# Optimization experiments

Measured on AMD Instinct MI355X. Metric: run time of the kernel, lower is better.

Reference implementation:

```python
import jax, jax.numpy as jnp
import numpy as np

N, n, m, k = 100000, 32, 16, 32
MU = 100.0  # bubble kernel scale (init arg mu)


def setup_inputs() -> dict:
    key = jax.random.key(0)
    ks = jax.random.split(key, 7)
    x = jax.random.normal(ks[0], (N,), dtype=jnp.float32)
    # torch.nn.Linear(N, n): weight [n, N], bias [n]
    encoder_w = jax.random.normal(ks[1], (n, N), dtype=jnp.float32) / np.float32(np.sqrt(N))
    encoder_b = jnp.zeros((n,), dtype=jnp.float32)
    # decoder parameter [n, N]
    decoder = jax.random.normal(ks[2], (n, N), dtype=jnp.float32) / np.float32(np.sqrt(n))
    # torch.nn.Linear(n, n*m): weight [n*m, n], bias [n*m]
    bw_w = jax.random.normal(ks[3], (n * m, n), dtype=jnp.float32) / np.float32(np.sqrt(n))
    bw_b = jnp.zeros((n * m,), dtype=jnp.float32)
    neighbour_distance = jax.random.uniform(ks[4], (N, k), dtype=jnp.float32)
    neighbour_id = jax.random.randint(ks[5], (N, k), 0, N)
    clustering_labels = jax.random.randint(ks[6], (N,), 0, m)
    return {
        "x": x,
        "encoder_w": encoder_w,
        "encoder_b": encoder_b,
        "decoder": decoder,
        "bw_w": bw_w,
        "bw_b": bw_b,
        "neighbour_distance": neighbour_distance,
        "neighbour_id": neighbour_id,
        "clustering_labels": clustering_labels,
    }


def reference(x, encoder_w, encoder_b, decoder, bw_w, bw_b,
              neighbour_distance, neighbour_id, clustering_labels):
    # encode: [N] -> [n]
    encoded = x @ encoder_w.T + encoder_b
    # per-basis, per-cluster bandwidths: sigmoid(Linear)/60 -> [n, m] -> expand to [n, N]
    bandwidths = jax.nn.sigmoid(encoded @ bw_w.T + bw_b) / 60.0
    w = bandwidths.reshape(n, m)[:, clustering_labels]  # [n, N]
    # bubble window: relu(1 - d^2 / (w*mu)^2) -> [n, N, k]
    window = jax.nn.relu(1.0 - neighbour_distance[None, :, :] ** 2
                         / (w[:, :, None] * MU) ** 2)
    # normalization over axis 1 (the N axis), faithful to the source's dim=1
    window = window / jnp.sum(window, axis=1, keepdims=True)
    # gather decoder rows at neighbours, weight, reduce over k: [n, N]
    convolved_basis = jnp.sum(decoder[:, neighbour_id] * window, axis=-1)
    # [n] @ [n, N] -> [N]
    return encoded @ convolved_basis
```

## Files before the change

kernel.cpp:

```cpp
#include <hip/hip_runtime.h>
#include <hip/hip_fp16.h>

#define N_PTS 100000
#define MU_F  100.0f
#define BUCKET 8192

typedef unsigned int uint;
typedef _Float16 h2 __attribute__((ext_vector_type(2)));
typedef float f2 __attribute__((ext_vector_type(2)));

#define E_SCALE 16384.0f
#define E_SCALE_INV (1.0f / 16384.0f)

static __device__ inline h2 h2pack(float a, float b) {
    return __builtin_bit_cast(h2, __builtin_amdgcn_cvt_pkrtz(a, b));
}
static __device__ inline float fdot2f(h2 a, h2 b, float c) {
    return __builtin_amdgcn_fdot2(a, b, c, false);
}
static __device__ inline h2 h2fma(h2 a, h2 b, h2 c) {
#if __has_builtin(__builtin_elementwise_fma)
    return __builtin_elementwise_fma(a, b, c);
#else
    return a * b + c;
#endif
}
static __device__ inline h2 h2max(h2 a, h2 b) {
#if __has_builtin(__builtin_elementwise_max)
    return __builtin_elementwise_max(a, b);
#else
    h2 r;
    r.x = a.x > b.x ? a.x : b.x;
    r.y = a.y > b.y ? a.y : b.y;
    return r;
#endif
}

#define ENC_BLKS 256
#define SC_BLKS  98
#define TR_BLKS  1563
#define S_BLKS   1024

__global__ __launch_bounds__(256) void k_prep(const float* __restrict__ x,
                                              const float* __restrict__ encW,
                                              const float* __restrict__ encB,
                                              const int* __restrict__ labels,
                                              float* __restrict__ enc,
                                              int* __restrict__ gcur,
                                              int* __restrict__ perm) {
    int b = blockIdx.x;
    if (b < ENC_BLKS) {
        int row = b & 31;
        int chunk = b >> 5;
        const int CH = N_PTS / 8;
        int base = chunk * CH;
        const float4* W4 = reinterpret_cast<const float4*>(encW + (size_t)row * N_PTS + base);
        const float4* x4 = reinterpret_cast<const float4*>(x + base);
        const int nv = CH / 4;
        float acc = 0.f;
        for (int idx = threadIdx.x; idx < nv; idx += 256) {
            float4 w = W4[idx];
            float4 xv = x4[idx];
            acc += w.x * xv.x + w.y * xv.y + w.z * xv.z + w.w * xv.w;
        }
        #pragma unroll
        for (int off = 32; off > 0; off >>= 1) acc += __shfl_down(acc, off);
        __shared__ float sred[4];
        int wid = threadIdx.x >> 6;
        if ((threadIdx.x & 63) == 0) sred[wid] = acc;
        __syncthreads();
        if (threadIdx.x == 0) {
            float s = sred[0] + sred[1] + sred[2] + sred[3];
            if (chunk == 0) s += encB[row];
            atomicAdd(enc + row, s);
        }
    } else {
        __shared__ int lh[16], lbase[16], lcur[16];
        const int CHUNK = 1024;
        int start = (b - ENC_BLKS) * CHUNK;
        int end = min(start + CHUNK, N_PTS);
        if (threadIdx.x < 16) { lh[threadIdx.x] = 0; lcur[threadIdx.x] = 0; }
        __syncthreads();
        for (int j = start + threadIdx.x; j < end; j += 256)
            atomicAdd(&lh[labels[j]], 1);
        __syncthreads();
        if (threadIdx.x < 16)
            lbase[threadIdx.x] = threadIdx.x * BUCKET +
                                 atomicAdd(&gcur[threadIdx.x], lh[threadIdx.x]);
        __syncthreads();
        for (int j = start + threadIdx.x; j < end; j += 256) {
            int c = labels[j];
            int lpos = atomicAdd(&lcur[c], 1);
            perm[lbase[c] + lpos] = j;
        }
    }
}

__device__ inline void build_invC(const float* __restrict__ encL,
                                  const float* __restrict__ bw_w,
                                  const float* __restrict__ bw_b,
                                  float* __restrict__ invCL, int c) {
    if (threadIdx.x < 32) {
        int r = threadIdx.x * 16 + c;
        float z = bw_b[r];
        const float* wr = bw_w + r * 32;
        #pragma unroll
        for (int p = 0; p < 32; ++p) z = fmaf(encL[p], wr[p], z);
        float s = 1.f / (1.f + __expf(-z));
        float wmu = s * (MU_F / 60.0f);
        invCL[threadIdx.x] = 1.f / (wmu * wmu);
    }
}

__global__ __launch_bounds__(256, 4) void k_S_sorted(const float* __restrict__ enc_g,
                                                     const float* __restrict__ bw_w,
                                                     const float* __restrict__ bw_b,
                                                     const float* __restrict__ nd,
                                                     const int* __restrict__ perm,
                                                     const int* __restrict__ gcur,
                                                     float* __restrict__ S,
                                                     float* __restrict__ S_part,
                                                     const float* __restrict__ dec,
                                                     __half* __restrict__ decT) {
    int b = blockIdx.x;
    if (b >= S_BLKS) {
        __shared__ float tile[32][65];
        int j0 = (b - S_BLKS) * 64;
        int col = threadIdx.x & 63;
        int r0 = threadIdx.x >> 6;
        #pragma unroll
        for (int it = 0; it < 8; ++it) {
            int row = it * 4 + r0;
            int j = j0 + col;
            float v = (j < N_PTS) ? dec[(size_t)row * N_PTS + j] : 0.f;
            tile[row][col] = v;
        }
        __syncthreads();
        #pragma unroll
        for (int it = 0; it < 4; ++it) {
            int idx = it * 256 + threadIdx.x;
            int j = idx >> 4;
            int p = idx & 15;
            int jj = j0 + j;
            if (jj < N_PTS) {
                __half2 h = __halves2half2(__float2half(tile[2 * p][j]),
                                           __float2half(tile[2 * p + 1][j]));
                *reinterpret_cast<__half2*>(decT + (size_t)jj * 32 + 2 * p) = h;
            }
        }
        return;
    }

    __shared__ float encL[32], invCL[32];
    __shared__ float Sloc[1024];
    int c = b & 15;
    int ch = b >> 4;
    if (threadIdx.x < 32) encL[threadIdx.x] = enc_g[threadIdx.x];
    for (int t = threadIdx.x; t < 1024; t += 256) Sloc[t] = 0.f;
    __syncthreads();
    build_invC(encL, bw_w, bw_b, invCL, c);
    __syncthreads();

    f2 inv2[16];
    #pragma unroll
    for (int t = 0; t < 16; ++t) { inv2[t].x = invCL[2 * t]; inv2[t].y = invCL[2 * t + 1]; }

    int bs = c * BUCKET;
    int cnt = gcur[c];
    int lane = threadIdx.x & 63;
    int kk = lane & 31;
    int jh = lane >> 5;
    int gw = ch * 4 + (threadIdx.x >> 6);
    const int nw = 64 * 4;
    int npairs = (cnt + 1) >> 1;

    f2 acc2[16];
    #pragma unroll
    for (int t = 0; t < 16; ++t) { acc2[t].x = 0.f; acc2[t].y = 0.f; }

    if (gw < npairs) {
        auto ld = [&](int pc, float& d, bool& v) {
            bool ok = pc < npairs;
            v = ok && (2 * pc + jh) < cnt;
            int p = v ? (bs + 2 * pc + jh) : bs;
            int j = __builtin_nontemporal_load(&perm[p]);
            d = __builtin_nontemporal_load(&nd[(size_t)j * 32 + kk]);
        };
        int pp = gw;
        float dA, dB; bool vA, vB;
        ld(pp, dA, vA);
        ld(pp + nw, dB, vB);
        while (pp < npairs) {
            float dC; bool vC;
            ld(pp + 2 * nw, dC, vC);
            float d2 = vA ? dA * dA : 1e30f;
            f2 md2; md2.x = -d2; md2.y = -d2;
            f2 onev; onev.x = 1.f; onev.y = 1.f;
            #pragma unroll
            for (int t = 0; t < 16; ++t) {
                f2 w = md2 * inv2[t] + onev;
                w.x = fmaxf(w.x, 0.f);
                w.y = fmaxf(w.y, 0.f);
                acc2[t] += w;
            }
            dA = dB; vA = vB; dB = dC; vB = vC;
            pp += nw;
        }
    }
    #pragma unroll
    for (int t = 0; t < 16; ++t) {
        acc2[t].x += __shfl_xor(acc2[t].x, 32);
        acc2[t].y += __shfl_xor(acc2[t].y, 32);
    }
    if (jh == 0) {
        #pragma unroll
        for (int t = 0; t < 16; ++t) {
            atomicAdd(&Sloc[(2 * t) * 32 + kk], acc2[t].x);
            atomicAdd(&Sloc[(2 * t + 1) * 32 + kk], acc2[t].y);
        }
    }
    __syncthreads();
    if (S_part) {
        for (int t = threadIdx.x; t < 1024; t += 256)
            S_part[(size_t)b * 1024 + t] = Sloc[t];
    } else {
        for (int t = threadIdx.x; t < 1024; t += 256) {
            float v = Sloc[t];
            if (v != 0.f) atomicAdd(&S[t], v);
        }
    }
}

__global__ __launch_bounds__(1024) void k_S_reduce(const float* __restrict__ S_part,
                                                   float* __restrict__ S) {
    int g = blockIdx.x;
    int t = threadIdx.x;
    float s = 0.f;
    #pragma unroll
    for (int u = 0; u < 16; ++u)
        s += S_part[(size_t)(g * 16 + u) * 1024 + t];
    atomicAdd(&S[t], s);
}

__global__ __launch_bounds__(256, 4) void k_main(const float* __restrict__ enc_g,
                                                 const float* __restrict__ bw_w,
                                                 const float* __restrict__ bw_b,
                                                 const float* __restrict__ S_g,
                                                 const float* __restrict__ nd,
                                                 const int* __restrict__ nid,
                                                 const int* __restrict__ perm,
                                                 const int* __restrict__ gcur,
                                                 const __half* __restrict__ decT,
                                                 float* __restrict__ out) {
    __shared__ float encL[32], invCL[32];
    __shared__ float ELf[1024];
    int c = blockIdx.x & 15;
    int ch = blockIdx.x >> 4;
    if (threadIdx.x < 32) encL[threadIdx.x] = enc_g[threadIdx.x];
    __syncthreads();
    build_invC(encL, bw_w, bw_b, invCL, c);
    for (int t = threadIdx.x; t < 1024; t += 256)
        ELf[t] = encL[t >> 5] / S_g[t] * E_SCALE;
    __syncthreads();

    int lane = threadIdx.x & 63;
    int R = lane >> 2;
    int q = lane & 3;

    h2 invh[4], EhA[4], EhB[4];
    #pragma unroll
    for (int t = 0; t < 4; ++t) {
        int i0 = q * 8 + 2 * t;
        invh[t] = h2pack(fminf(invCL[i0], 6.0e4f), fminf(invCL[i0 + 1], 6.0e4f));
        EhA[t] = h2pack(ELf[i0 * 32 + R], ELf[(i0 + 1) * 32 + R]);
        EhB[t] = h2pack(ELf[i0 * 32 + R + 16], ELf[(i0 + 1) * 32 + R + 16]);
    }
    const h2 zero2 = h2pack(0.f, 0.f);
    const h2 one2 = h2pack(1.f, 1.f);

    int bs = c * BUCKET;
    int cnt = gcur[c];
    int wv = ch * 4 + (threadIdx.x >> 6);
    const int NW = 64 * 4;
    int npairs = (cnt + 1) >> 1;
    const uint4* decQ = reinterpret_cast<const uint4*>(decT);
    if (wv >= npairs) return;

    auto load_pair = [&](int pp, int& j0, int& j1, bool& v1) {
        bool ok = pp < npairs;
        int p0 = ok ? (bs + 2 * pp) : bs;
        v1 = ok && ((2 * pp + 1) < cnt);
        j0 = perm[p0];
        j1 = perm[v1 ? p0 + 1 : p0];
    };
    auto load_ids = [&](int j0, int j1, int* id, float* dd) {
        #pragma unroll
        for (int s = 0; s < 4; ++s) {
            int jj = (s >> 1) ? j1 : j0;
            size_t idx = (size_t)jj * 32 + (s & 1) * 16 + R;
            id[s] = __builtin_nontemporal_load(&nid[idx]);
            dd[s] = __builtin_nontemporal_load(&nd[idx]);
        }
    };
    auto load_rows = [&](const int* id, uint4* r) {
        #pragma unroll
        for (int s = 0; s < 4; ++s)
            r[s] = decQ[(size_t)id[s] * 4 + q];
    };

    int pp = wv;
    int j0a, j1a, j0b, j1b, j0c, j1c; bool v1a, v1b, v1c;
    int ida[4], idn[4]; float dda[4], ddn[4];
    uint4 ra[4], rb[4];

    load_pair(pp, j0a, j1a, v1a);
    load_ids(j0a, j1a, ida, dda);
    load_pair(pp + NW, j0b, j1b, v1b);
    load_rows(ida, ra);
    load_ids(j0b, j1b, idn, ddn);
    load_pair(pp + 2 * NW, j0c, j1c, v1c);

    while (pp < npairs) {
        load_rows(idn, rb);
        int idc[4]; float ddc[4];
        load_ids(j0c, j1c, idc, ddc);
        int j0d, j1d; bool v1d;
        load_pair(pp + 3 * NW, j0d, j1d, v1d);

        float d20 = dda[0] * dda[0];
        float d21 = dda[1] * dda[1];
        float d22 = dda[2] * dda[2];
        float d23 = dda[3] * dda[3];
        h2 md0 = h2pack(-d20, -d20);
        h2 md1 = h2pack(-d21, -d21);
        h2 md2 = h2pack(-d22, -d22);
        h2 md3 = h2pack(-d23, -d23);

        float a0 = 0.f, a1 = 0.f, a2 = 0.f, a3 = 0.f;
        #pragma unroll
        for (int t = 0; t < 4; ++t) {
            uint dw0 = (t == 0) ? ra[0].x : (t == 1) ? ra[0].y : (t == 2) ? ra[0].z : ra[0].w;
            uint dw1 = (t == 0) ? ra[1].x : (t == 1) ? ra[1].y : (t == 2) ? ra[1].z : ra[1].w;
            uint dw2 = (t == 0) ? ra[2].x : (t == 1) ? ra[2].y : (t == 2) ? ra[2].z : ra[2].w;
            uint dw3 = (t == 0) ? ra[3].x : (t == 1) ? ra[3].y : (t == 2) ? ra[3].z : ra[3].w;
            {
                h2 w = h2max(h2fma(md0, invh[t], one2), zero2);
                a0 = fdot2f(w * EhA[t], __builtin_bit_cast(h2, dw0), a0);
            }
            {
                h2 w = h2max(h2fma(md1, invh[t], one2), zero2);
                a1 = fdot2f(w * EhB[t], __builtin_bit_cast(h2, dw1), a1);
            }
            {
                h2 w = h2max(h2fma(md2, invh[t], one2), zero2);
                a2 = fdot2f(w * EhA[t], __builtin_bit_cast(h2, dw2), a2);
            }
            {
                h2 w = h2max(h2fma(md3, invh[t], one2), zero2);
                a3 = fdot2f(w * EhB[t], __builtin_bit_cast(h2, dw3), a3);
            }
        }
        float u = a0 + a1;
        float v = a2 + a3;
        #pragma unroll
        for (int off = 32; off > 0; off >>= 1) {
            u += __shfl_xor(u, off);
            v += __shfl_xor(v, off);
        }
        if (lane == 0) out[j0a] = u * E_SCALE_INV;
        if (lane == 32 && v1a) out[j1a] = v * E_SCALE_INV;

        j0a = j0b; j1a = j1b; v1a = v1b;
        j0b = j0c; j1b = j1c; v1b = v1c;
        j0c = j0d; j1c = j1d; v1c = v1d;
        #pragma unroll
        for (int s = 0; s < 4; ++s) {
            dda[s] = ddn[s];
            ddn[s] = ddc[s];
            idn[s] = idc[s];
            ra[s] = rb[s];
        }
        pp += NW;
    }
}

extern "C" void kernel_launch(void* const* d_in, const int* in_sizes, int n_in,
                              void* d_out, int out_size, void* d_ws, size_t ws_size,
                              hipStream_t stream) {
    const float* x     = (const float*)d_in[0];
    const float* enc_w = (const float*)d_in[1];
    const float* enc_b = (const float*)d_in[2];
    const float* dec   = (const float*)d_in[3];
    const float* bw_w  = (const float*)d_in[4];
    const float* bw_b  = (const float*)d_in[5];
    const float* nd    = (const float*)d_in[6];
    const int*   nid   = (const int*)d_in[7];
    const int*   labels= (const int*)d_in[8];
    float* out = (float*)d_out;

    char* ws = (char*)d_ws;
    float* enc    = (float*)(ws + 0);
    float* S      = (float*)(ws + 128);
    int* gcur     = (int*)(ws + 4224);
    int* perm     = (int*)(ws + 8192);
    __half* decT  = (__half*)(ws + 532480);
    bool use_part = ws_size >= 11126784ull;
    float* S_part = use_part ? (float*)(ws + 6932480) : nullptr;

    (void)hipMemsetAsync(d_ws, 0, 4288, stream);
    k_prep<<<dim3(ENC_BLKS + SC_BLKS), dim3(256), 0, stream>>>(
        x, enc_w, enc_b, labels, enc, gcur, perm);
    k_S_sorted<<<dim3(S_BLKS + TR_BLKS), dim3(256), 0, stream>>>(
        enc, bw_w, bw_b, nd, perm, gcur, S, S_part, dec, decT);
    if (use_part)
        k_S_reduce<<<dim3(64), dim3(1024), 0, stream>>>(S_part, S);
    k_main<<<dim3(1024), dim3(256), 0, stream>>>(enc, bw_w, bw_b, S, nd, nid,
                                                 perm, gcur, decT, out);
}
```

Measured before the change: 180.2 us.

## Drop cluster-label sort; index per-point bandwidths from shared table in natural order

Removes the counting-sort permutation by cluster label and its per-bucket work distribution. Both the S-reduction and the main kernel now walk points in their natural order in contiguous chunks, and they look up each point's inverse bandwidths from a 16x32 shared-memory table indexed by label. This gets rid of the perm indirection, the sort work in k_prep and the label-imbalanced buckets, and makes the nd/nid loads contiguous. The cost is per-point shared-memory table reads that depend on the label, plus the full 512-entry bandwidth computation in every block.

```diff
diff --git a/kernel.cpp b/kernel.cpp
--- a/kernel.cpp
+++ b/kernel.cpp
@@ -3,7 +3,6 @@
 
 #define N_PTS 100000
 #define MU_F  100.0f
-#define BUCKET 8192
 
 typedef unsigned int uint;
 typedef _Float16 h2 __attribute__((ext_vector_type(2)));
@@ -37,91 +36,69 @@
 }
 
 #define ENC_BLKS 256
-#define SC_BLKS  98
 #define TR_BLKS  1563
 #define S_BLKS   1024
+#define NPAIRS   (N_PTS / 2)
+#define S_CH     ((NPAIRS + S_BLKS - 1) / S_BLKS)
+#define M_BLKS   1024
+#define M_CH     ((NPAIRS + M_BLKS - 1) / M_BLKS)
 
 __global__ __launch_bounds__(256) void k_prep(const float* __restrict__ x,
                                               const float* __restrict__ encW,
                                               const float* __restrict__ encB,
-                                              const int* __restrict__ labels,
-                                              float* __restrict__ enc,
-                                              int* __restrict__ gcur,
-                                              int* __restrict__ perm) {
+                                              float* __restrict__ enc) {
     int b = blockIdx.x;
-    if (b < ENC_BLKS) {
-        int row = b & 31;
-        int chunk = b >> 5;
-        const int CH = N_PTS / 8;
-        int base = chunk * CH;
-        const float4* W4 = reinterpret_cast<const float4*>(encW + (size_t)row * N_PTS + base);
-        const float4* x4 = reinterpret_cast<const float4*>(x + base);
-        const int nv = CH / 4;
-        float acc = 0.f;
-        for (int idx = threadIdx.x; idx < nv; idx += 256) {
-            float4 w = W4[idx];
-            float4 xv = x4[idx];
-            acc += w.x * xv.x + w.y * xv.y + w.z * xv.z + w.w * xv.w;
-        }
-        #pragma unroll
-        for (int off = 32; off > 0; off >>= 1) acc += __shfl_down(acc, off);
-        __shared__ float sred[4];
-        int wid = threadIdx.x >> 6;
-        if ((threadIdx.x & 63) == 0) sred[wid] = acc;
-        __syncthreads();
-        if (threadIdx.x == 0) {
-            float s = sred[0] + sred[1] + sred[2] + sred[3];
-            if (chunk == 0) s += encB[row];
-            atomicAdd(enc + row, s);
-        }
-    } else {
-        __shared__ int lh[16], lbase[16], lcur[16];
-        const int CHUNK = 1024;
-        int start = (b - ENC_BLKS) * CHUNK;
-        int end = min(start + CHUNK, N_PTS);
-        if (threadIdx.x < 16) { lh[threadIdx.x] = 0; lcur[threadIdx.x] = 0; }
-        __syncthreads();
-        for (int j = start + threadIdx.x; j < end; j += 256)
-            atomicAdd(&lh[labels[j]], 1);
-        __syncthreads();
-        if (threadIdx.x < 16)
-            lbase[threadIdx.x] = threadIdx.x * BUCKET +
-                                 atomicAdd(&gcur[threadIdx.x], lh[threadIdx.x]);
-        __syncthreads();
-        for (int j = start + threadIdx.x; j < end; j += 256) {
-            int c = labels[j];
-            int lpos = atomicAdd(&lcur[c], 1);
-            perm[lbase[c] + lpos] = j;
-        }
-    }
-}
-
-__device__ inline void build_invC(const float* __restrict__ encL,
+    int row = b & 31;
+    int chunk = b >> 5;
+    const int CH = N_PTS / 8;
+    int base = chunk * CH;
+    const float4* W4 = reinterpret_cast<const float4*>(encW + (size_t)row * N_PTS + base);
+    const float4* x4 = reinterpret_cast<const float4*>(x + base);
+    const int nv = CH / 4;
+    float acc = 0.f;
+    for (int idx = threadIdx.x; idx < nv; idx += 256) {
+        float4 w = W4[idx];
+        float4 xv = x4[idx];
+        acc += w.x * xv.x + w.y * xv.y + w.z * xv.z + w.w * xv.w;
+    }
+    #pragma unroll
+    for (int off = 32; off > 0; off >>= 1) acc += __shfl_down(acc, off);
+    __shared__ float sred[4];
+    int wid = threadIdx.x >> 6;
+    if ((threadIdx.x & 63) == 0) sred[wid] = acc;
+    __syncthreads();
+    if (threadIdx.x == 0) {
+        float s = sred[0] + sred[1] + sred[2] + sred[3];
+        if (chunk == 0) s += encB[row];
+        atomicAdd(enc + row, s);
+    }
+}
+
+__device__ inline void build_invF(const float* __restrict__ encL,
                                   const float* __restrict__ bw_w,
                                   const float* __restrict__ bw_b,
-                                  float* __restrict__ invCL, int c) {
-    if (threadIdx.x < 32) {
-        int r = threadIdx.x * 16 + c;
+                                  float* __restrict__ invF) {
+    for (int r = threadIdx.x; r < 512; r += 256) {
+        int i = r >> 4, c = r & 15;
         float z = bw_b[r];
         const float* wr = bw_w + r * 32;
         #pragma unroll
         for (int p = 0; p < 32; ++p) z = fmaf(encL[p], wr[p], z);
         float s = 1.f / (1.f + __expf(-z));
         float wmu = s * (MU_F / 60.0f);
-        invCL[threadIdx.x] = 1.f / (wmu * wmu);
-    }
-}
-
-__global__ __launch_bounds__(256, 4) void k_S_sorted(const float* __restrict__ enc_g,
-                                                     const float* __restrict__ bw_w,
-                                                     const float* __restrict__ bw_b,
-                                                     const float* __restrict__ nd,
-                                                     const int* __restrict__ perm,
-                                                     const int* __restrict__ gcur,
-                                                     float* __restrict__ S,
-                                                     float* __restrict__ S_part,
-                                                     const float* __restrict__ dec,
-                                                     __half* __restrict__ decT) {
+        invF[c * 32 + i] = 1.f / (wmu * wmu);
+    }
+}
+
+__global__ __launch_bounds__(256, 4) void k_S(const float* __restrict__ enc_g,
+                                              const float* __restrict__ bw_w,
+                                              const float* __restrict__ bw_b,
+                                              const float* __restrict__ nd,
+                                              const int* __restrict__ labels,
+                                              float* __restrict__ S,
+                                              float* __restrict__ S_part,
+                                              const float* __restrict__ dec,
+                                              __half* __restrict__ decT) {
     int b = blockIdx.x;
     if (b >= S_BLKS) {
         __shared__ float tile[32][65];
@@ -151,60 +128,60 @@
         return;
     }
 
-    __shared__ float encL[32], invCL[32];
+    __shared__ float encL[32];
+    __shared__ float invF[512];
     __shared__ float Sloc[1024];
-    int c = b & 15;
-    int ch = b >> 4;
     if (threadIdx.x < 32) encL[threadIdx.x] = enc_g[threadIdx.x];
     for (int t = threadIdx.x; t < 1024; t += 256) Sloc[t] = 0.f;
     __syncthreads();
-    build_invC(encL, bw_w, bw_b, invCL, c);
-    __syncthreads();
-
-    f2 inv2[16];
-    #pragma unroll
-    for (int t = 0; t < 16; ++t) { inv2[t].x = invCL[2 * t]; inv2[t].y = invCL[2 * t + 1]; }
-
-    int bs = c * BUCKET;
-    int cnt = gcur[c];
+    build_invF(encL, bw_w, bw_b, invF);
+    __syncthreads();
+
     int lane = threadIdx.x & 63;
     int kk = lane & 31;
     int jh = lane >> 5;
-    int gw = ch * 4 + (threadIdx.x >> 6);
-    const int nw = 64 * 4;
-    int npairs = (cnt + 1) >> 1;
+    int w = threadIdx.x >> 6;
+    int start = b * S_CH;
+    int pend = min(start + S_CH, NPAIRS);
+    int p = start + w;
 
     f2 acc2[16];
     #pragma unroll
     for (int t = 0; t < 16; ++t) { acc2[t].x = 0.f; acc2[t].y = 0.f; }
 
-    if (gw < npairs) {
-        auto ld = [&](int pc, float& d, bool& v) {
-            bool ok = pc < npairs;
-            v = ok && (2 * pc + jh) < cnt;
-            int p = v ? (bs + 2 * pc + jh) : bs;
-            int j = __builtin_nontemporal_load(&perm[p]);
-            d = __builtin_nontemporal_load(&nd[(size_t)j * 32 + kk]);
+    if (p < pend) {
+        auto ld = [&](int pc, float& d, int& c) {
+            pc = min(pc, NPAIRS - 1);
+            int j = 2 * pc + jh;
+            d = nd[(size_t)j * 32 + kk];
+            c = labels[j];
         };
-        int pp = gw;
-        float dA, dB; bool vA, vB;
-        ld(pp, dA, vA);
-        ld(pp + nw, dB, vB);
-        while (pp < npairs) {
-            float dC; bool vC;
-            ld(pp + 2 * nw, dC, vC);
-            float d2 = vA ? dA * dA : 1e30f;
+        float dA, dB; int cA, cB;
+        ld(p, dA, cA);
+        ld(p + 4, dB, cB);
+        f2 onev; onev.x = 1.f; onev.y = 1.f;
+        while (p < pend) {
+            float dC; int cC;
+            ld(p + 8, dC, cC);
+            float d2 = dA * dA;
             f2 md2; md2.x = -d2; md2.y = -d2;
-            f2 onev; onev.x = 1.f; onev.y = 1.f;
+            const float4* ivp = reinterpret_cast<const float4*>(&invF[cA * 32]);
             #pragma unroll
-            for (int t = 0; t < 16; ++t) {
-                f2 w = md2 * inv2[t] + onev;
-                w.x = fmaxf(w.x, 0.f);
-                w.y = fmaxf(w.y, 0.f);
-                acc2[t] += w;
-            }
-            dA = dB; vA = vB; dB = dC; vB = vC;
-            pp += nw;
+            for (int t4 = 0; t4 < 8; ++t4) {
+                float4 iv = ivp[t4];
+                f2 i01; i01.x = iv.x; i01.y = iv.y;
+                f2 i23; i23.x = iv.z; i23.y = iv.w;
+                f2 w0 = md2 * i01 + onev;
+                w0.x = fmaxf(w0.x, 0.f);
+                w0.y = fmaxf(w0.y, 0.f);
+                acc2[2 * t4] += w0;
+                f2 w1 = md2 * i23 + onev;
+                w1.x = fmaxf(w1.x, 0.f);
+                w1.y = fmaxf(w1.y, 0.f);
+                acc2[2 * t4 + 1] += w1;
+            }
+            dA = dB; cA = cB; dB = dC; cB = cC;
+            p += 4;
         }
     }
     #pragma unroll
@@ -248,84 +225,92 @@
                                                  const float* __restrict__ S_g,
                                                  const float* __restrict__ nd,
                                                  const int* __restrict__ nid,
-                                                 const int* __restrict__ perm,
-                                                 const int* __restrict__ gcur,
+                                                 const int* __restrict__ labels,
                                                  const __half* __restrict__ decT,
                                                  float* __restrict__ out) {
-    __shared__ float encL[32], invCL[32];
+    __shared__ float encL[32];
+    __shared__ float invF[512];
     __shared__ float ELf[1024];
-    int c = blockIdx.x & 15;
-    int ch = blockIdx.x >> 4;
+    __shared__ h2 invHL[256];
+
     if (threadIdx.x < 32) encL[threadIdx.x] = enc_g[threadIdx.x];
     __syncthreads();
-    build_invC(encL, bw_w, bw_b, invCL, c);
+    build_invF(encL, bw_w, bw_b, invF);
     for (int t = threadIdx.x; t < 1024; t += 256)
         ELf[t] = encL[t >> 5] / S_g[t] * E_SCALE;
+    __syncthreads();
+    {
+        int t = threadIdx.x;
+        int c = t >> 4, q = (t >> 2) & 3, tt = t & 3;
+        int i0 = q * 8 + 2 * tt;
+        invHL[t] = h2pack(fminf(invF[c * 32 + i0], 6.0e4f),
+                          fminf(invF[c * 32 + i0 + 1], 6.0e4f));
+    }
     __syncthreads();
 
     int lane = threadIdx.x & 63;
     int R = lane >> 2;
     int q = lane & 3;
 
-    h2 invh[4], EhA[4], EhB[4];
+    h2 EhA[4], EhB[4];
     #pragma unroll
     for (int t = 0; t < 4; ++t) {
         int i0 = q * 8 + 2 * t;
-        invh[t] = h2pack(fminf(invCL[i0], 6.0e4f), fminf(invCL[i0 + 1], 6.0e4f));
         EhA[t] = h2pack(ELf[i0 * 32 + R], ELf[(i0 + 1) * 32 + R]);
         EhB[t] = h2pack(ELf[i0 * 32 + R + 16], ELf[(i0 + 1) * 32 + R + 16]);
     }
     const h2 zero2 = h2pack(0.f, 0.f);
     const h2 one2 = h2pack(1.f, 1.f);
 
-    int bs = c * BUCKET;
-    int cnt = gcur[c];
-    int wv = ch * 4 + (threadIdx.x >> 6);
-    const int NW = 64 * 4;
-    int npairs = (cnt + 1) >> 1;
+    int w = threadIdx.x >> 6;
+    int start = blockIdx.x * M_CH;
+    int pend = min(start + M_CH, NPAIRS);
+    int pa = start + w;
     const uint4* decQ = reinterpret_cast<const uint4*>(decT);
-    if (wv >= npairs) return;
-
-    auto load_pair = [&](int pp, int& j0, int& j1, bool& v1) {
-        bool ok = pp < npairs;
-        int p0 = ok ? (bs + 2 * pp) : bs;
-        v1 = ok && ((2 * pp + 1) < cnt);
-        j0 = perm[p0];
-        j1 = perm[v1 ? p0 + 1 : p0];
-    };
-    auto load_ids = [&](int j0, int j1, int* id, float* dd) {
+    if (pa >= pend) return;
+
+    auto load_ldd = [&](int pc, int* id, float* dd, int& c0, int& c1) {
+        pc = min(pc, NPAIRS - 1);
+        int j0 = 2 * pc, j1 = j0 + 1;
         #pragma unroll
         for (int s = 0; s < 4; ++s) {
-            int jj = (s >> 1) ? j1 : j0;
-            size_t idx = (size_t)jj * 32 + (s & 1) * 16 + R;
-            id[s] = __builtin_nontemporal_load(&nid[idx]);
-            dd[s] = __builtin_nontemporal_load(&nd[idx]);
-        }
+            size_t idx = (size_t)((s >> 1) ? j1 : j0) * 32 + (s & 1) * 16 + R;
+            id[s] = nid[idx];
+            dd[s] = nd[idx];
+        }
+        c0 = labels[j0];
+        c1 = labels[j1];
     };
     auto load_rows = [&](const int* id, uint4* r) {
         #pragma unroll
         for (int s = 0; s < 4; ++s)
             r[s] = decQ[(size_t)id[s] * 4 + q];
     };
-
-    int pp = wv;
-    int j0a, j1a, j0b, j1b, j0c, j1c; bool v1a, v1b, v1c;
-    int ida[4], idn[4]; float dda[4], ddn[4];
+    auto load_ih = [&](int c0, int c1, h2* ih0, h2* ih1) {
+        uint4 a = *reinterpret_cast<const uint4*>(&invHL[c0 * 16 + q * 4]);
+        uint4 bq = *reinterpret_cast<const uint4*>(&invHL[c1 * 16 + q * 4]);
+        ih0[0] = __builtin_bit_cast(h2, a.x);  ih0[1] = __builtin_bit_cast(h2, a.y);
+        ih0[2] = __builtin_bit_cast(h2, a.z);  ih0[3] = __builtin_bit_cast(h2, a.w);
+        ih1[0] = __builtin_bit_cast(h2, bq.x); ih1[1] = __builtin_bit_cast(h2, bq.y);
+        ih1[2] = __builtin_bit_cast(h2, bq.z); ih1[3] = __builtin_bit_cast(h2, bq.w);
+    };
+
+    int ida[4], idb[4]; float dda[4], ddb[4];
+    int ca0, ca1, cb0, cb1;
     uint4 ra[4], rb[4];
-
-    load_pair(pp, j0a, j1a, v1a);
-    load_ids(j0a, j1a, ida, dda);
-    load_pair(pp + NW, j0b, j1b, v1b);
+    h2 ihA0[4], ihA1[4];
+
+    load_ldd(pa, ida, dda, ca0, ca1);
+    load_ldd(pa + 4, idb, ddb, cb0, cb1);
     load_rows(ida, ra);
-    load_ids(j0b, j1b, idn, ddn);
-    load_pair(pp + 2 * NW, j0c, j1c, v1c);
-
-    while (pp < npairs) {
-        load_rows(idn, rb);
-        int idc[4]; float ddc[4];
-        load_ids(j0c, j1c, idc, ddc);
-        int j0d, j1d; bool v1d;
-        load_pair(pp + 3 * NW, j0d, j1d, v1d);
+    load_ih(ca0, ca1, ihA0, ihA1);
+
+    while (pa < pend) {
+        load_rows(idb, rb);
+        h2 ihB0[4], ihB1[4];
+        load_ih(cb0, cb1, ihB0, ihB1);
+        int idc[4]; float ddc[4]; int cc0, cc1;
+        load_ldd(pa + 8, idc, ddc, cc0, cc1);
 
         float d20 = dda[0] * dda[0];
         float d21 = dda[1] * dda[1];
@@ -344,20 +329,20 @@
             uint dw2 = (t == 0) ? ra[2].x : (t == 1) ? ra[2].y : (t == 2) ? ra[2].z : ra[2].w;
             uint dw3 = (t == 0) ? ra[3].x : (t == 1) ? ra[3].y : (t == 2) ? ra[3].z : ra[3].w;
             {
-                h2 w = h2max(h2fma(md0, invh[t], one2), zero2);
-                a0 = fdot2f(w * EhA[t], __builtin_bit_cast(h2, dw0), a0);
+                h2 wv = h2max(h2fma(md0, ihA0[t], one2), zero2);
+                a0 = fdot2f(wv * EhA[t], __builtin_bit_cast(h2, dw0), a0);
             }
             {
-                h2 w = h2max(h2fma(md1, invh[t], one2), zero2);
-                a1 = fdot2f(w * EhB[t], __builtin_bit_cast(h2, dw1), a1);
+                h2 wv = h2max(h2fma(md1, ihA0[t], one2), zero2);
+                a1 = fdot2f(wv * EhB[t], __builtin_bit_cast(h2, dw1), a1);
             }
             {
-                h2 w = h2max(h2fma(md2, invh[t], one2), zero2);
-                a2 = fdot2f(w * EhA[t], __builtin_bit_cast(h2, dw2), a2);
+                h2 wv = h2max(h2fma(md2, ihA1[t], one2), zero2);
+                a2 = fdot2f(wv * EhA[t], __builtin_bit_cast(h2, dw2), a2);
             }
             {
-                h2 w = h2max(h2fma(md3, invh[t], one2), zero2);
-                a3 = fdot2f(w * EhB[t], __builtin_bit_cast(h2, dw3), a3);
+                h2 wv = h2max(h2fma(md3, ihA1[t], one2), zero2);
+                a3 = fdot2f(wv * EhB[t], __builtin_bit_cast(h2, dw3), a3);
             }
         }
         float u = a0 + a1;
@@ -367,20 +352,18 @@
             u += __shfl_xor(u, off);
             v += __shfl_xor(v, off);
         }
-        if (lane == 0) out[j0a] = u * E_SCALE_INV;
-        if (lane == 32 && v1a) out[j1a] = v * E_SCALE_INV;
-
-        j0a = j0b; j1a = j1b; v1a = v1b;
-        j0b = j0c; j1b = j1c; v1b = v1c;
-        j0c = j0d; j1c = j1d; v1c = v1d;
+        if (lane == 0)  out[2 * pa]     = u * E_SCALE_INV;
+        if (lane == 32) out[2 * pa + 1] = v * E_SCALE_INV;
+
+        ca0 = cb0; ca1 = cb1; cb0 = cc0; cb1 = cc1;
         #pragma unroll
         for (int s = 0; s < 4; ++s) {
-            dda[s] = ddn[s];
-            ddn[s] = ddc[s];
-            idn[s] = idc[s];
+            dda[s] = ddb[s]; ddb[s] = ddc[s];
+            ida[s] = idb[s]; idb[s] = idc[s];
             ra[s] = rb[s];
-        }
-        pp += NW;
+            ihA0[s] = ihB0[s]; ihA1[s] = ihB1[s];
+        }
+        pa += 4;
     }
 }
 
@@ -401,19 +384,16 @@
     char* ws = (char*)d_ws;
     float* enc    = (float*)(ws + 0);
     float* S      = (float*)(ws + 128);
-    int* gcur     = (int*)(ws + 4224);
-    int* perm     = (int*)(ws + 8192);
     __half* decT  = (__half*)(ws + 532480);
     bool use_part = ws_size >= 11126784ull;
     float* S_part = use_part ? (float*)(ws + 6932480) : nullptr;
 
-    (void)hipMemsetAsync(d_ws, 0, 4288, stream);
-    k_prep<<<dim3(ENC_BLKS + SC_BLKS), dim3(256), 0, stream>>>(
-        x, enc_w, enc_b, labels, enc, gcur, perm);
-    k_S_sorted<<<dim3(S_BLKS + TR_BLKS), dim3(256), 0, stream>>>(
-        enc, bw_w, bw_b, nd, perm, gcur, S, S_part, dec, decT);
+    (void)hipMemsetAsync(d_ws, 0, 4224, stream);
+    k_prep<<<dim3(ENC_BLKS), dim3(256), 0, stream>>>(x, enc_w, enc_b, enc);
+    k_S<<<dim3(S_BLKS + TR_BLKS), dim3(256), 0, stream>>>(
+        enc, bw_w, bw_b, nd, labels, S, S_part, dec, decT);
     if (use_part)
         k_S_reduce<<<dim3(64), dim3(1024), 0, stream>>>(S_part, S);
-    k_main<<<dim3(1024), dim3(256), 0, stream>>>(enc, bw_w, bw_b, S, nd, nid,
-                                                 perm, gcur, decT, out);
-}
+    k_main<<<dim3(M_BLKS), dim3(256), 0, stream>>>(enc, bw_w, bw_b, S, nd, nid,
+                                                   labels, decT, out);
+}
```

After: 190.9 us. +6.0%, slower.
